# Performance work log

Measured on AMD Instinct MI355X. Metric: run time of the kernel, lower is better.

The kernel has to match this reference:

```python
import jax, jax.numpy as jnp
from jax import lax
import numpy as np

B, H, W = 8, 96, 96
CIN, COUT, QD, NH = 256, 128, 32, 8
LA_MID = COUT // 8  # 16
GRIDS = (6, 3, 2, 1)
EPS = 1e-5  # torch BatchNorm default eps


def conv2d(x, w):
    # 'same' padding for 3x3 stride 1 (autopad k//2)
    return lax.conv_general_dilated(x, w, (1, 1), 'SAME',
                                    dimension_numbers=('NCHW', 'OIHW', 'NCHW'))


def bn2d(x, g, b, m, v):
    inv = g / jnp.sqrt(v + EPS)
    return x * inv[None, :, None, None] + (b - m * inv)[None, :, None, None]


def adaptive_avg_pool_tokens(x, oh, ow):
    # matches torch adaptive_avg_pool2d bin edges; returns [b, c, oh*ow]
    b, c, h, w = x.shape
    cells = []
    for i in range(oh):
        h0, h1 = (i * h) // oh, -((-(i + 1) * h) // oh)
        for j in range(ow):
            w0, w1 = (j * w) // ow, -((-(j + 1) * w) // ow)
            cells.append(x[:, :, h0:h1, w0:w1].mean(axis=(2, 3)))
    return jnp.stack(cells, axis=-1)


def psp(x, grids):
    b, c, h, w = x.shape
    ar = w / h
    return jnp.concatenate(
        [adaptive_avg_pool_tokens(x, g, max(1, round(ar * g))) for g in grids], axis=2)


def setup_inputs() -> dict:
    key = jax.random.key(0)
    ks = jax.random.split(key, 9)
    f = jnp.float32
    return {
        'x': jax.random.normal(ks[0], (B, CIN, H, W), f),
        'w_red': jax.random.normal(ks[1], (COUT, CIN, 3, 3), f) * 0.02,
        'bng': jnp.ones((COUT,), f), 'bnb': jnp.zeros((COUT,), f),
        'bnm': jnp.zeros((COUT,), f), 'bnv': jnp.ones((COUT,), f),
        'w_q': jax.random.normal(ks[2], (QD, COUT), f) * 0.1,
        'b_q': jnp.zeros((QD,), f),
        'w_k': jax.random.normal(ks[3], (QD, COUT), f) * 0.1,
        'b_k': jnp.zeros((QD,), f),
        'w_v': jax.random.normal(ks[4], (COUT, COUT), f) * 0.08,
        'b_v': jnp.zeros((COUT,), f),
        'lsh': jax.random.normal(ks[5], (NH, QD), f),
        'w_la1': jax.random.normal(ks[6], (LA_MID, COUT), f) * 0.1,
        'lag': jnp.ones((LA_MID,), f), 'lab': jnp.zeros((LA_MID,), f),
        'lam': jnp.zeros((LA_MID,), f), 'lav': jnp.ones((LA_MID,), f),
        'w_la2': jax.random.normal(ks[7], (COUT, LA_MID, 3, 3), f) * 0.02,
    }


def reference(x, w_red, bng, bnb, bnm, bnv, w_q, b_q, w_k, b_k, w_v, b_v,
              lsh, w_la1, lag, lab, lam, lav, w_la2):
    # reduce_channel: Conv(256,128,3) = conv + BN + SiLU
    xr = jax.nn.silu(bn2d(conv2d(x, w_red), bng, bnb, bnm, bnv))  # [B,COUT,H,W]
    b, c, h, w = xr.shape
    # query: 1x1 conv to 32 ch, flatten spatial -> [B, HW, QD]
    q = (jnp.einsum('oc,bchw->bohw', w_q, xr)
         + b_q[None, :, None, None]).reshape(b, QD, h * w).transpose(0, 2, 1)
    # key_psp and value_psp act on the same xr -> identical token sets [B,COUT,50]
    tokens = psp(xr, GRIDS)
    k_tok = (jnp.einsum('oc,bcn->bon', w_k, tokens)
             + b_k[None, :, None]).transpose(0, 2, 1)  # [B,50,QD]
    v_tok = (jnp.einsum('oc,bcn->bon', w_v, tokens)
             + b_v[None, :, None]).transpose(0, 2, 1)  # [B,50,COUT]
    # ReformerAttention: argmax over TOKEN dim -> [B, NH]; sort indices lie in [0,NH)
    # so the gather picks a per-batch permutation of the first NH key/value tokens
    # (faithful to the torch code; q_buckets is computed but unused there).
    k_buckets = jnp.argmax(jnp.einsum('hd,bnd->bhn', lsh, k_tok), axis=-1)  # [B,NH]
    k_idx = jnp.argsort(k_buckets, axis=-1)  # [B,NH], values in [0,NH)
    k_s = jnp.take_along_axis(k_tok, k_idx[:, :, None], axis=1)  # [B,NH,QD]
    v_s = jnp.take_along_axis(v_tok, k_idx[:, :, None], axis=1)  # [B,NH,COUT]
    att = jax.nn.softmax(jnp.einsum('bqd,bkd->bqk', q, k_s), axis=-1)  # [B,HW,NH]
    ctx = jnp.einsum('bqk,bkd->bqd', att, v_s).transpose(0, 2, 1).reshape(b, COUT, h, w)
    # LocalAttenModule: Conv(128,16,1)(conv+bn+silu) -> 3x3 conv 16->128 -> tanh mask
    y = jax.nn.silu(bn2d(jnp.einsum('oc,bchw->bohw', w_la1, ctx), lag, lab, lam, lav))
    mask = jnp.tanh(conv2d(y, w_la2))
    ctx = ctx * mask + ctx
    return xr + ctx
```

## Files before the change

kernel.cpp:

```cpp
#include <hip/hip_runtime.h>
#include <hip/hip_bf16.h>
#include <cmath>

typedef __attribute__((ext_vector_type(8))) short short8;
typedef __attribute__((ext_vector_type(4))) short s16x4;
typedef __attribute__((ext_vector_type(4))) float f32x4;
typedef unsigned short u16;

#define HW 9216

__device__ inline float bf2f(u16 u) {
    union { unsigned int i; float f; } x; x.i = ((unsigned int)u) << 16; return x.f;
}
__device__ inline u16 f2bf(float f) {
    union { unsigned int i; float f; } x; x.f = f;
    unsigned int r = x.i + 0x7FFF + ((x.i >> 16) & 1);
    return (u16)(r >> 16);
}

__device__ inline void gload16(const u16* g, u16* l) {
    __builtin_amdgcn_global_load_lds(
        (const __attribute__((address_space(1))) void*)g,
        (__attribute__((address_space(3))) void*)l,
        16, 0, 0);
}

__global__ __launch_bounds__(256) void transform_w(
    const float* __restrict__ wred, const float* __restrict__ wla2,
    u16* __restrict__ Wt1, u16* __restrict__ Wt2)
{
    int idx = blockIdx.x * 256 + threadIdx.x;
    if (idx < 128 * 2304) {
        int co = idx / 2304;
        int rem = idx - co * 2304;
        int c = rem / 288;
        int r2 = rem - c * 288;
        int khw = r2 >> 5, ciL = r2 & 31;
        Wt1[idx] = f2bf(wred[((co * 256 + c * 32 + ciL) * 9 + khw)]);
    } else {
        int i2 = idx - 128 * 2304;
        if (i2 < 128 * 160) {
            int co = i2 / 160;
            int k = i2 - co * 160;
            int khw = k >> 4, ci = k & 15;
            Wt2[i2] = (khw < 9) ? f2bf(wla2[((co << 4) + ci) * 9 + khw]) : (u16)0;
        }
    }
}

__global__ __launch_bounds__(256) void transpose_x(
    const float* __restrict__ X, u16* __restrict__ Xt)
{
    int bid = blockIdx.x;
    int b = bid & 7, chunk = bid >> 3;
    int p = chunk * 256 + threadIdx.x;
    const float* xb = X + (size_t)b * 256 * HW + p;
    u16* ot = Xt + ((size_t)b * HW + p) * 256;
    for (int oct = 0; oct < 32; ++oct) {
        short8 v;
#pragma unroll
        for (int j = 0; j < 8; ++j)
            v[j] = (short)f2bf(xb[(size_t)(oct * 8 + j) * HW]);
        *(short8*)(ot + oct * 8) = v;
    }
}

template<int CIN, int KTILES, int KP, int EPI>
__global__ __launch_bounds__(256) void conv_k(
    const u16* __restrict__ Xt, const u16* __restrict__ Wt,
    u16* OutH, float* OutF,
    const float* __restrict__ bg, const float* __restrict__ bb,
    const float* __restrict__ bm, const float* __restrict__ bv,
    const u16* __restrict__ xrb, const float* ctxf,
    const u16* __restrict__ zp)
{
    __shared__ __align__(16) short As[2][128 * 32];
    __shared__ __align__(16) short Bs[2][96 * 32];
    __shared__ float invA[128], betA[128];

    const int tid = threadIdx.x;
    const int bid = blockIdx.x;
    const int b = bid & 7;
    const int tile = bid >> 3;
    const int w0 = (tile % 3) * 32;
    const int h0 = (tile / 3) * 3;

    const int lane = tid & 63;
    const int wid = tid >> 6;
    const int wm = (wid & 1) * 64;
    const int wn = (wid >> 1) * 48;
    const int r = lane & 15;
    const int quad = lane >> 4;

    if constexpr (EPI == 1) {
        if (tid < 128) {
            float iv = bg[tid] * rsqrtf(bv[tid] + 1e-5f);
            invA[tid] = iv;
            betA[tid] = bb[tid] - bm[tid] * iv;
        }
    }

    const u16* XtB = Xt + (size_t)b * HW * CIN;

    auto bsrc = [&](int slot, int kt) -> const u16* {
        int row = slot >> 2, o = slot & 3;
        int pw = row & 31, ph = row >> 5;
        int hgl = h0 + ph, wgl = w0 + pw;
        if (CIN == 256) {
            int c = (kt * 57) >> 9;
            int khw = kt - c * 9;
            int dh = (khw * 11) >> 5;
            int dw = khw - 3 * dh;
            int hh = hgl + dh - 1, ww = wgl + dw - 1;
            bool ok = ((unsigned)hh < 96u) && ((unsigned)ww < 96u);
            return ok ? XtB + ((size_t)hh * 96 + ww) * 256 + c * 32 + o * 8 : zp;
        } else {
            int kg = kt * 32 + o * 8;
            int khw = kg >> 4, ci0 = kg & 15;
            int dh = (khw * 11) >> 5, dw = khw - 3 * dh;
            int hh = hgl + dh - 1, ww = wgl + dw - 1;
            bool ok = ((unsigned)hh < 96u) && ((unsigned)ww < 96u) && (khw < 9);
            return ok ? XtB + ((size_t)hh * 96 + ww) * 16 + ci0 : zp;
        }
    };

    auto stage = [&](int kt, int buf) {
        int sA0 = tid, sA1 = tid + 256;
        gload16(Wt + (size_t)(sA0 >> 2) * KP + kt * 32 + (sA0 & 3) * 8,
                (u16*)&As[buf][(64 * wid) * 8]);
        gload16(Wt + (size_t)(sA1 >> 2) * KP + kt * 32 + (sA1 & 3) * 8,
                (u16*)&As[buf][(256 + 64 * wid) * 8]);
        gload16(bsrc(tid, kt), (u16*)&Bs[buf][(64 * wid) * 8]);
        if (wid < 2)
            gload16(bsrc(tid + 256, kt), (u16*)&Bs[buf][(256 + 64 * wid) * 8]);
    };

    f32x4 acc[4][3];
    f32x4 zz = {0.f, 0.f, 0.f, 0.f};
#pragma unroll
    for (int i = 0; i < 4; i++)
#pragma unroll
        for (int j = 0; j < 3; j++) acc[i][j] = zz;

    stage(0, 0);
    __syncthreads();

    for (int kt = 0; kt < KTILES; ++kt) {
        int cur = kt & 1;
        if (kt + 1 < KTILES) stage(kt + 1, cur ^ 1);
        short8 af[4], bfr[3];
#pragma unroll
        for (int i = 0; i < 4; i++)
            af[i] = *(const short8*)(&As[cur][(wm + i * 16 + r) * 32 + quad * 8]);
#pragma unroll
        for (int j = 0; j < 3; j++)
            bfr[j] = *(const short8*)(&Bs[cur][(wn + j * 16 + r) * 32 + quad * 8]);
        __builtin_amdgcn_s_setprio(1);
#pragma unroll
        for (int i = 0; i < 4; i++)
#pragma unroll
            for (int j = 0; j < 3; j++)
                acc[i][j] = __builtin_amdgcn_mfma_f32_16x16x32_bf16(af[i], bfr[j], acc[i][j], 0, 0, 0);
        __builtin_amdgcn_s_setprio(0);
        if (kt + 1 < KTILES)
            __syncthreads();
    }

#pragma unroll
    for (int i = 0; i < 4; i++) {
#pragma unroll
        for (int j = 0; j < 3; j++) {
            int pl = wn + j * 16 + r;
            int w = w0 + (pl & 31), h = h0 + (pl >> 5);
#pragma unroll
            for (int g = 0; g < 4; ++g) {
                int co = wm + i * 16 + quad * 4 + g;
                float v = acc[i][j][g];
                size_t oidx = ((size_t)b * 128 + co) * HW + h * 96 + w;
                if constexpr (EPI == 1) {
                    float val = v * invA[co] + betA[co];
                    float sv = val / (1.f + __expf(-val));
                    OutH[oidx] = f2bf(sv);
                } else {
                    float xv = bf2f(xrb[oidx]);
                    float cv = ctxf[oidx];
                    float e = __expf(2.f * v);
                    float th = 1.f - 2.f / (e + 1.f);
                    OutF[oidx] = xv + cv * (1.f + th);
                }
            }
        }
    }
}

__global__ __launch_bounds__(256) void prep_attn(
    const u16* __restrict__ xr,
    const float* __restrict__ wk, const float* __restrict__ bk,
    const float* __restrict__ wv, const float* __restrict__ bv,
    const float* __restrict__ wq, const float* __restrict__ bq,
    float* __restrict__ Aout, float* __restrict__ Vout, float* __restrict__ c0out)
{
    __shared__ float part[256];
    __shared__ float tok[128];
    __shared__ float ks[32];
    int t = threadIdx.x;
    int bid = blockIdx.x;
    int b = bid & 7, n = bid >> 3;
    int c = t & 127, half = t >> 7;
    int i0 = (n < 6) ? 0 : 16;
    int j0 = ((n < 6) ? n : (n - 6)) * 16;
    const u16* xb = xr + (size_t)(b * 128 + c) * HW;

    float s = 0.f;
    for (int rr = 0; rr < 8; ++rr) {
        int row = i0 + half * 8 + rr;
        const u16* rp = xb + row * 96 + j0;
        short8 v0 = *(const short8*)rp;
        short8 v1 = *(const short8*)(rp + 8);
#pragma unroll
        for (int j = 0; j < 8; ++j) s += bf2f((u16)v0[j]) + bf2f((u16)v1[j]);
    }
    part[t] = s;
    __syncthreads();
    if (t < 128) tok[t] = (part[t] + part[t + 128]) * (1.f / 256.f);
    __syncthreads();
    if (t < 32) {
        float s2 = bk[t];
        for (int cc = 0; cc < 128; ++cc) s2 += wk[t * 128 + cc] * tok[cc];
        ks[t] = s2;
    }
    __syncthreads();
    if (t < 128) {
        float s3 = bv[c];
        for (int c2 = 0; c2 < 128; ++c2) s3 += wv[c * 128 + c2] * tok[c2];
        Vout[((size_t)b * 8 + n) * 128 + c] = s3;
    } else {
        float s4 = 0.f;
        for (int d = 0; d < 32; ++d) s4 += wq[d * 128 + c] * ks[d];
        Aout[((size_t)b * 8 + n) * 128 + c] = s4;
    }
    if (t == 0) {
        float s5 = 0.f;
        for (int d = 0; d < 32; ++d) s5 += bq[d] * ks[d];
        c0out[b * 8 + n] = s5;
    }
}

__global__ __launch_bounds__(256) void attn_k(
    const u16* __restrict__ xr,
    const float* __restrict__ Ain, const float* __restrict__ Vin,
    const float* __restrict__ c0in,
    const float* __restrict__ wla1,
    const float* __restrict__ lag, const float* __restrict__ lab,
    const float* __restrict__ lam, const float* __restrict__ lav,
    float* __restrict__ ctxout, u16* __restrict__ yout)
{
    __shared__ float Xs[128 * 64];
    __shared__ float As[8 * 128], Vs[8 * 128], Ws[16 * 128];
    __shared__ float satt[8 * 64];
    __shared__ float c0s[8], inv1[16], bet1[16];

    int t = threadIdx.x;
    int bid = blockIdx.x;
    int b = bid & 7;
    int p0 = (bid >> 3) * 64;

    for (int i = t; i < 1024; i += 256) { As[i] = Ain[b * 1024 + i]; Vs[i] = Vin[b * 1024 + i]; }
    for (int i = t; i < 2048; i += 256) Ws[i] = wla1[i];
    if (t < 8) c0s[t] = c0in[b * 8 + t];
    if (t < 16) {
        float iv = lag[t] * rsqrtf(lav[t] + 1e-5f);
        inv1[t] = iv; bet1[t] = lab[t] - lam[t] * iv;
    }
    const u16* xb = xr + (size_t)b * 128 * HW + p0;
#pragma unroll
    for (int it = 0; it < 4; ++it) {
        int c = (t >> 3) + it * 32;
        int seg = t & 7;
        short8 v = *(const short8*)(xb + (size_t)c * HW + seg * 8);
#pragma unroll
        for (int j = 0; j < 8; ++j) Xs[c * 64 + seg * 8 + j] = bf2f((u16)v[j]);
    }
    __syncthreads();
    {
        int pp = t & 63, ng = t >> 6;
        float a0 = 0.f, a1 = 0.f;
        for (int c = 0; c < 128; ++c) {
            float x = Xs[c * 64 + pp];
            a0 += As[(ng * 2) * 128 + c] * x;
            a1 += As[(ng * 2 + 1) * 128 + c] * x;
        }
        satt[(ng * 2) * 64 + pp] = a0 + c0s[ng * 2];
        satt[(ng * 2 + 1) * 64 + pp] = a1 + c0s[ng * 2 + 1];
    }
    __syncthreads();
    if (t < 64) {
        float m = -1e30f;
        float sv[8];
#pragma unroll
        for (int n = 0; n < 8; ++n) { sv[n] = satt[n * 64 + t]; m = fmaxf(m, sv[n]); }
        float sum = 0.f;
#pragma unroll
        for (int n = 0; n < 8; ++n) { sv[n] = __expf(sv[n] - m); sum += sv[n]; }
        float rcp = 1.f / sum;
#pragma unroll
        for (int n = 0; n < 8; ++n) satt[n * 64 + t] = sv[n] * rcp;
    }
    __syncthreads();
    {
        int pp = t & 63, cg = t >> 6;
        float at[8];
#pragma unroll
        for (int n = 0; n < 8; ++n) at[n] = satt[n * 64 + pp];
        for (int ci = 0; ci < 32; ++ci) {
            int c = cg * 32 + ci;
            float s = 0.f;
#pragma unroll
            for (int n = 0; n < 8; ++n) s += at[n] * Vs[n * 128 + c];
            ctxout[((size_t)b * 128 + c) * HW + p0 + pp] = s;
            Xs[c * 64 + pp] = s;
        }
    }
    __syncthreads();
    {
        int pp = t & 63, dg = t >> 6;
        float a[4] = {0.f, 0.f, 0.f, 0.f};
        for (int c = 0; c < 128; ++c) {
            float x = Xs[c * 64 + pp];
#pragma unroll
            for (int k = 0; k < 4; ++k) a[k] += Ws[(dg * 4 + k) * 128 + c] * x;
        }
        s16x4 pk;
#pragma unroll
        for (int k = 0; k < 4; ++k) {
            int d = dg * 4 + k;
            float val = a[k] * inv1[d] + bet1[d];
            float s = val / (1.f + __expf(-val));
            pk[k] = (short)f2bf(s);
        }
        *(s16x4*)(yout + ((size_t)b * HW + p0 + pp) * 16 + dg * 4) = pk;
    }
}

extern "C" void kernel_launch(void* const* d_in, const int* in_sizes, int n_in,
                              void* d_out, int out_size, void* d_ws, size_t ws_size,
                              hipStream_t stream)
{
    const float* x    = (const float*)d_in[0];
    const float* wred = (const float*)d_in[1];
    const float* bng  = (const float*)d_in[2];
    const float* bnb  = (const float*)d_in[3];
    const float* bnm  = (const float*)d_in[4];
    const float* bnv  = (const float*)d_in[5];
    const float* wq   = (const float*)d_in[6];
    const float* bq   = (const float*)d_in[7];
    const float* wk   = (const float*)d_in[8];
    const float* bk   = (const float*)d_in[9];
    const float* wv   = (const float*)d_in[10];
    const float* bv   = (const float*)d_in[11];
    const float* wla1 = (const float*)d_in[13];
    const float* lag  = (const float*)d_in[14];
    const float* lab  = (const float*)d_in[15];
    const float* lam  = (const float*)d_in[16];
    const float* lav  = (const float*)d_in[17];
    const float* wla2 = (const float*)d_in[18];

    char* ws = (char*)d_ws;
    u16*   xr  = (u16*)(ws + 0);
    u16*   yt  = (u16*)(ws + 18874368);
    u16*   Wt1 = (u16*)(ws + 21233664);
    u16*   Wt2 = (u16*)(ws + 21823488);
    float* Ab  = (float*)(ws + 21864448);
    float* Vb  = (float*)(ws + 21897216);
    float* c0b = (float*)(ws + 21929984);
    u16*   xt   = (u16*)d_out;
    float* outp = (float*)d_out;
    const u16* zp = Wt2 + 144;

    transform_w<<<dim3(1232), dim3(256), 0, stream>>>(wred, wla2, Wt1, Wt2);

    transpose_x<<<dim3(288), dim3(256), 0, stream>>>(x, xt);

    conv_k<256, 72, 2304, 1><<<dim3(768), dim3(256), 0, stream>>>(
        xt, Wt1, xr, nullptr, bng, bnb, bnm, bnv, nullptr, nullptr, zp);

    prep_attn<<<dim3(64), dim3(256), 0, stream>>>(xr, wk, bk, wv, bv, wq, bq, Ab, Vb, c0b);

    attn_k<<<dim3(1152), dim3(256), 0, stream>>>(
        xr, Ab, Vb, c0b, wla1, lag, lab, lam, lav, outp, yt);

    conv_k<16, 5, 160, 2><<<dim3(768), dim3(256), 0, stream>>>(
        yt, Wt2, nullptr, outp, nullptr, nullptr, nullptr, nullptr, xr, outp, zp);
}
```

Measured before the change: 309.4 us.

## Load conv weight fragments directly into registers instead of staging through LDS

```diff
diff --git a/kernel.cpp b/kernel.cpp
--- a/kernel.cpp
+++ b/kernel.cpp
@@ -74,7 +74,6 @@
     const u16* __restrict__ xrb, const float* ctxf,
     const u16* __restrict__ zp)
 {
-    __shared__ __align__(16) short As[2][128 * 32];
     __shared__ __align__(16) short Bs[2][96 * 32];
     __shared__ float invA[128], betA[128];
 
@@ -124,17 +123,19 @@
         }
     };
 
-    auto stage = [&](int kt, int buf) {
-        int sA0 = tid, sA1 = tid + 256;
-        gload16(Wt + (size_t)(sA0 >> 2) * KP + kt * 32 + (sA0 & 3) * 8,
-                (u16*)&As[buf][(64 * wid) * 8]);
-        gload16(Wt + (size_t)(sA1 >> 2) * KP + kt * 32 + (sA1 & 3) * 8,
-                (u16*)&As[buf][(256 + 64 * wid) * 8]);
+    auto stageB = [&](int kt, int buf) {
         gload16(bsrc(tid, kt), (u16*)&Bs[buf][(64 * wid) * 8]);
         if (wid < 2)
             gload16(bsrc(tid + 256, kt), (u16*)&Bs[buf][(256 + 64 * wid) * 8]);
     };
 
+    const u16* Arow = Wt + (size_t)(wm + r) * KP + quad * 8;
+    auto loadA = [&](int kt, short8* dst) {
+#pragma unroll
+        for (int i = 0; i < 4; i++)
+            dst[i] = *(const short8*)(Arow + (size_t)i * 16 * KP + kt * 32);
+    };
+
     f32x4 acc[4][3];
     f32x4 zz = {0.f, 0.f, 0.f, 0.f};
 #pragma unroll
@@ -142,16 +143,8 @@
 #pragma unroll
         for (int j = 0; j < 3; j++) acc[i][j] = zz;
 
-    stage(0, 0);
-    __syncthreads();
-
-    for (int kt = 0; kt < KTILES; ++kt) {
-        int cur = kt & 1;
-        if (kt + 1 < KTILES) stage(kt + 1, cur ^ 1);
-        short8 af[4], bfr[3];
-#pragma unroll
-        for (int i = 0; i < 4; i++)
-            af[i] = *(const short8*)(&As[cur][(wm + i * 16 + r) * 32 + quad * 8]);
+    auto compute = [&](int cur, short8* af) {
+        short8 bfr[3];
 #pragma unroll
         for (int j = 0; j < 3; j++)
             bfr[j] = *(const short8*)(&Bs[cur][(wn + j * 16 + r) * 32 + quad * 8]);
@@ -162,8 +155,23 @@
             for (int j = 0; j < 3; j++)
                 acc[i][j] = __builtin_amdgcn_mfma_f32_16x16x32_bf16(af[i], bfr[j], acc[i][j], 0, 0, 0);
         __builtin_amdgcn_s_setprio(0);
-        if (kt + 1 < KTILES)
+    };
+
+    short8 aA[4], aB[4];
+
+    loadA(0, aA);
+    stageB(0, 0);
+    __syncthreads();
+
+    for (int kt = 0; kt < KTILES; kt += 2) {
+        if (kt + 1 < KTILES) { loadA(kt + 1, aB); stageB(kt + 1, 1); }
+        compute(0, aA);
+        if (kt + 1 < KTILES) {
             __syncthreads();
+            if (kt + 2 < KTILES) { loadA(kt + 2, aA); stageB(kt + 2, 0); }
+            compute(1, aB);
+            if (kt + 2 < KTILES) __syncthreads();
+        }
     }
 
 #pragma unroll
```

After: 369.3 us. 19.4% more time.
